# Optimization experiments

Hardware: AMD Instinct MI355X
Metric: run time of the kernel (lower is better)

The kernel has to match this reference:

```python
import jax, jax.numpy as jnp
from jax import lax
import numpy as np

STRIDE = 4
RADIUS = 0.2
NSAMPLE = 32
DENSITY_K = 16
INTRINSIC_DIM = 3
EPS = 1e-8
BN_EPS = 1e-5


def _cdist(a, b):
    # Euclidean pairwise distances: a (..., M, 3), b (..., N, 3) -> (..., M, N)
    d2 = ((a * a).sum(-1)[..., :, None] + (b * b).sum(-1)[..., None, :]
          - 2.0 * jnp.matmul(a, jnp.swapaxes(b, -1, -2)))
    return jnp.sqrt(jnp.maximum(d2, 1e-12))


def _fps(coords, n_samples):
    # iterative farthest point sampling: coords (B, N, 3) -> (B, n_samples) int32
    B, N, _ = coords.shape
    mean = coords.mean(axis=1, keepdims=True)
    farthest = jnp.argmax(((coords - mean) ** 2).sum(-1), axis=1)
    min_dist = jnp.full((B, N), jnp.inf, dtype=coords.dtype)

    def step(carry, _):
        md, far = carry
        centroid = jnp.take_along_axis(coords, far[:, None, None], axis=1)  # (B,1,3)
        d = ((coords - centroid) ** 2).sum(-1)
        md = jnp.minimum(md, d)
        return (md, jnp.argmax(md, axis=1)), far

    _, idxs = lax.scan(step, (min_dist, farthest), None, length=n_samples)
    return idxs.T  # (B, n_samples)


def _ball_query(q, s, radius, k):
    d = _cdist(q, s)  # (B, M, N)
    _, knn_idx = lax.top_k(-d, k)                 # k nearest fallback
    masked = jnp.where(d > radius, jnp.inf, d)
    neg_vals, m_idx = lax.top_k(-masked, k)       # k nearest within radius
    valid = jnp.isfinite(neg_vals)
    return jnp.where(valid, m_idx, knn_idx)


def _density_weights(gc):
    # gc: (B, M, K, 3) -> weights (B, M, K); kth-NN-distance based density weights
    K = gc.shape[2]
    d = _cdist(gc, gc)  # (B, M, K, K)
    d = jnp.where(jnp.eye(K, dtype=bool), jnp.inf, d)
    kk = min(max(DENSITY_K, 1), K - 1)
    kth = -lax.top_k(-d, kk)[0][..., -1]  # distance to kk-th neighbor, (B, M, K)
    raw = jnp.maximum(kth, EPS) ** INTRINSIC_DIM
    return raw / jnp.maximum(raw.sum(axis=-1, keepdims=True), EPS)


def _bn(x, g, b, axes):
    # training-mode batchnorm (biased variance), channel axis = 1
    mu = x.mean(axes, keepdims=True)
    var = x.var(axes, keepdims=True)
    shp = [1] * x.ndim
    shp[1] = -1
    return (x - mu) / jnp.sqrt(var + BN_EPS) * g.reshape(shp) + b.reshape(shp)


def setup_inputs() -> dict:
    key = jax.random.key(0)
    ks = jax.random.split(key, 5)
    B, N, C_in, C_out = 8, 4096, 64, 128
    mid = C_out // 2  # stride > 1 -> mid_channels = out_channels // 2
    coords = jax.random.uniform(ks[0], (B, N, 3), dtype=jnp.float32)
    feats = jax.random.normal(ks[1], (B, C_in, N), dtype=jnp.float32)
    W0 = jax.random.normal(ks[2], (mid, C_in + 3), dtype=jnp.float32) * 0.05
    W1 = jax.random.normal(ks[3], (C_out, mid), dtype=jnp.float32) * 0.05
    Ws = jax.random.normal(ks[4], (C_out, C_in), dtype=jnp.float32) * 0.05
    return {
        "coords": coords, "feats": feats,
        "W0": W0, "g0": jnp.ones((mid,), jnp.float32), "b0": jnp.zeros((mid,), jnp.float32),
        "W1": W1, "g1": jnp.ones((C_out,), jnp.float32), "b1": jnp.zeros((C_out,), jnp.float32),
        "Ws": Ws, "gs": jnp.ones((C_out,), jnp.float32), "bs": jnp.zeros((C_out,), jnp.float32),
    }


def reference(coords, feats, W0, g0, b0, W1, g1, b1, Ws, gs, bs):
    B, N, _ = coords.shape
    M = max(N // STRIDE, 1)
    sample_idx = _fps(coords, M)                               # (B, M)
    gather_pts = jax.vmap(lambda c, i: c[i])                   # (N,3)[idx]
    gather_fts = jax.vmap(lambda f, i: f[:, i])                # (C,N)[:,idx]
    sampled_coords = gather_pts(coords, sample_idx)            # (B, M, 3)
    gidx = _ball_query(sampled_coords, coords, RADIUS, NSAMPLE)  # (B, M, K)
    grouped_coords = gather_pts(coords, gidx)                  # (B, M, K, 3)
    rel = (grouped_coords - sampled_coords[:, :, None, :]) / max(RADIUS, 1e-8)
    grouped_feats = gather_fts(feats, gidx)                    # (B, C_in, M, K)
    x = jnp.concatenate([rel.transpose(0, 3, 1, 2), grouped_feats], axis=1)
    h = jax.nn.relu(_bn(jnp.einsum('oc,bcmk->bomk', W0, x), g0, b0, (0, 2, 3)))
    messages = jax.nn.relu(_bn(jnp.einsum('oc,bcmk->bomk', W1, h), g1, b1, (0, 2, 3)))
    weights = _density_weights(grouped_coords)                 # (B, M, K)
    reduced = (messages * weights[:, None, :, :]).sum(-1)      # (B, C_out, M)
    skip_in = gather_fts(feats, sample_idx)                    # (B, C_in, M)
    skip = _bn(jnp.einsum('oc,bcm->bom', Ws, skip_in), gs, bs, (0, 2))
    return sampled_coords, jax.nn.relu(reduced + skip)
```

## Files before the change

kernel.cpp:

```cpp
#include <hip/hip_runtime.h>
#include <hip/hip_bf16.h>
#include <cstdint>

#define DEV __device__ __forceinline__

constexpr int Bn   = 8;
constexpr int Nn   = 4096;
constexpr int Mn   = 1024;
constexpr int Kn   = 32;
constexpr int CIN  = 64;
constexpr int COUT = 128;

__global__ __launch_bounds__(256) void k_tr(const float* __restrict__ feats,
                                            float* __restrict__ featsT) {
  __shared__ float tile[64][65];
  int b = blockIdx.x >> 6, n0 = (blockIdx.x & 63) * 64;
  int t = threadIdx.x;
  int lane = t & 63, grp = t >> 6;
  for (int r = 0; r < 16; ++r) {
    int c = grp + r * 4;
    tile[c][lane] = feats[((size_t)b * 64 + c) * 4096 + n0 + lane];
  }
  __syncthreads();
  for (int r = 0; r < 16; ++r) {
    int n = grp + r * 4;
    featsT[((size_t)b * 4096 + n0 + n) * 64 + lane] = tile[lane][n];
  }
}

DEV float wave_max_f32(float x) {
#if __has_builtin(__builtin_amdgcn_update_dpp)
#define FSTEP(CTRL, RMASK)                                                      \
  {                                                                             \
    int o = __builtin_amdgcn_update_dpp(0, __float_as_int(x), CTRL, RMASK, 0xf, \
                                        false);                                 \
    x = fmaxf(x, __int_as_float(o));                                            \
  }
  FSTEP(0x111, 0xf)
  FSTEP(0x112, 0xf)
  FSTEP(0x114, 0xf)
  FSTEP(0x118, 0xf)
  FSTEP(0x142, 0xa)
  FSTEP(0x143, 0xc)
#undef FSTEP
#else
  for (int off = 1; off < 64; off <<= 1) x = fmaxf(x, __shfl_xor(x, off, 64));
#endif
  return x;
}

DEV unsigned long long grp8_max_u64(unsigned long long k) {
#if __has_builtin(__builtin_amdgcn_update_dpp)
#define USTEP(CTRL)                                                                    \
  {                                                                                    \
    unsigned int lo = (unsigned int)__builtin_amdgcn_update_dpp(                       \
        0, (int)(unsigned int)k, CTRL, 0xf, 0xf, false);                               \
    unsigned int hi = (unsigned int)__builtin_amdgcn_update_dpp(                       \
        0, (int)(unsigned int)(k >> 32), CTRL, 0xf, 0xf, false);                       \
    unsigned long long o = ((unsigned long long)hi << 32) | lo;                        \
    if (o > k) k = o;                                                                  \
  }
  USTEP(0x111)
  USTEP(0x112)
  USTEP(0x114)
#undef USTEP
#else
  for (int off = 1; off < 8; off <<= 1) {
    unsigned int lo = __shfl_xor((unsigned int)k, off, 64);
    unsigned int hi = __shfl_xor((unsigned int)(k >> 32), off, 64);
    unsigned long long o = ((unsigned long long)hi << 32) | lo;
    if (o > k) k = o;
  }
#endif
  return k;
}

DEV uint32_t fps_round8(const float v[8], int t, unsigned long long (*part)[8], int p) {
  float v4[4]; int j4[4];
#pragma unroll
  for (int i = 0; i < 4; ++i) {
    bool r = v[2 * i + 1] > v[2 * i];
    v4[i] = r ? v[2 * i + 1] : v[2 * i];
    j4[i] = r ? 2 * i + 1 : 2 * i;
  }
  float v2[2]; int j2[2];
#pragma unroll
  for (int i = 0; i < 2; ++i) {
    bool r = v4[2 * i + 1] > v4[2 * i];
    v2[i] = r ? v4[2 * i + 1] : v4[2 * i];
    j2[i] = r ? j4[2 * i + 1] : j4[2 * i];
  }
  bool rr = v2[1] > v2[0];
  float bv = rr ? v2[1] : v2[0];
  int bj = rr ? j2[1] : j2[0];

  float wl = wave_max_f32(bv);
  float wmax = __int_as_float(__builtin_amdgcn_readlane(__float_as_int(wl), 63));
  unsigned long long mask = __ballot(bv == wmax);
  int Ls = (int)__ffsll(mask) - 1;
  int bjw = __shfl(bj, Ls, 64);
  uint32_t idx = 8u * (uint32_t)((t & ~63) + Ls) + (uint32_t)bjw;
  const int sl = p & 1;
  if ((t & 63) == 0)
    part[sl][t >> 6] = ((unsigned long long)__float_as_uint(wmax) << 12) |
                       (unsigned long long)(4095u - idx);
  __syncthreads();
  unsigned long long kk = part[sl][t & 7];
  kk = grp8_max_u64(kk);
  unsigned int lo = (unsigned int)__builtin_amdgcn_readlane((int)(unsigned int)kk, 7);
  return 4095u - (lo & 4095u);
}

__global__ __launch_bounds__(512, 1) void k_fps(const float* __restrict__ coords,
                                                uint32_t* __restrict__ sidx,
                                                float* __restrict__ outc) {
  const int b = blockIdx.x, t = threadIdx.x;
  __shared__ float4 sp[Nn];
  __shared__ unsigned long long part[2][8];
  __shared__ uint32_t farl[Mn];
  __shared__ float s_mean[4];

  const float* cb = coords + (size_t)b * Nn * 3;
  for (int i = t; i < Nn; i += 512)
    sp[i] = make_float4(cb[3 * i], cb[3 * i + 1], cb[3 * i + 2], 0.f);
  __syncthreads();
  if (t == 0) {
    float ax = 0.f, ay = 0.f, az = 0.f;
    for (int i = 0; i < Nn; ++i) {
      float4 c = sp[i];
      ax = __fadd_rn(ax, c.x); ay = __fadd_rn(ay, c.y); az = __fadd_rn(az, c.z);
    }
    s_mean[0] = __fdiv_rn(ax, 4096.f);
    s_mean[1] = __fdiv_rn(ay, 4096.f);
    s_mean[2] = __fdiv_rn(az, 4096.f);
  }
  __syncthreads();

  float px[8], py[8], pz[8], md[8];
#pragma unroll
  for (int j = 0; j < 8; ++j) {
    float4 c = sp[8 * t + j];
    px[j] = c.x; py[j] = c.y; pz[j] = c.z;
    md[j] = __builtin_inff();
  }

  uint32_t far;
  {
    float mx = s_mean[0], my = s_mean[1], mz = s_mean[2];
    float tv[8];
#pragma unroll
    for (int j = 0; j < 8; ++j) {
      float dx = __fsub_rn(px[j], mx), dy = __fsub_rn(py[j], my), dz = __fsub_rn(pz[j], mz);
      tv[j] = __fadd_rn(__fadd_rn(__fmul_rn(dx, dx), __fmul_rn(dy, dy)), __fmul_rn(dz, dz));
    }
    far = fps_round8(tv, t, part, 0);
  }

  for (int p = 1; p < Mn; ++p) {
    if (t == 0) farl[p - 1] = far;
    float4 c = sp[far];
#pragma unroll
    for (int j = 0; j < 8; ++j) {
      float dx = __fsub_rn(px[j], c.x), dy = __fsub_rn(py[j], c.y), dz = __fsub_rn(pz[j], c.z);
      float d = __fadd_rn(__fadd_rn(__fmul_rn(dx, dx), __fmul_rn(dy, dy)), __fmul_rn(dz, dz));
      md[j] = fminf(md[j], d);
    }
    far = fps_round8(md, t, part, p);
  }
  if (t == 0) farl[Mn - 1] = far;
  __syncthreads();

  for (int i = t; i < Mn; i += 512) {
    uint32_t f = farl[i];
    sidx[b * Mn + i] = f;
    float4 c = sp[f];
    outc[(size_t)(b * Mn + i) * 3 + 0] = c.x;
    outc[(size_t)(b * Mn + i) * 3 + 1] = c.y;
    outc[(size_t)(b * Mn + i) * 3 + 2] = c.z;
  }
}

__global__ __launch_bounds__(256) void k_knn(const float* __restrict__ coords,
                                             const uint32_t* __restrict__ sidx,
                                             uint32_t* __restrict__ gidx,
                                             float* __restrict__ wts) {
  const int q = blockIdx.x;
  const int b = q >> 10;
  const int t = threadIdx.x;
  __shared__ unsigned long long keys[Nn + 2];
  __shared__ int s_cnt;
  __shared__ float s_q[4];
  __shared__ uint32_t s_sel[32];
  __shared__ float gx[32], gy[32], gz[32], g2[32];
  __shared__ float dmat[32 * 33];
  __shared__ float kth[32];
  __shared__ float s_raw[32];
  __shared__ float s_sum;

  if (t == 0) {
    uint32_t si = sidx[q];
    const float* c = &coords[((size_t)b * Nn + si) * 3];
    s_q[0] = c[0]; s_q[1] = c[1]; s_q[2] = c[2];
  }
  __syncthreads();
  float qx = s_q[0], qy = s_q[1], qz = s_q[2];
  float q2 = __fadd_rn(__fadd_rn(__fmul_rn(qx, qx), __fmul_rn(qy, qy)), __fmul_rn(qz, qz));
  const float* cb = coords + (size_t)b * Nn * 3;

  float thr = 0.04f;
  int cnt = 0;
  while (true) {
    if (t == 0) s_cnt = 0;
    __syncthreads();
    for (int j = 0; j < 16; ++j) {
      int i = t + 256 * j;
      float cx = cb[3 * i], cy = cb[3 * i + 1], cz = cb[3 * i + 2];
      float c2  = __fadd_rn(__fadd_rn(__fmul_rn(cx, cx), __fmul_rn(cy, cy)), __fmul_rn(cz, cz));
      float dot = __fadd_rn(__fadd_rn(__fmul_rn(qx, cx), __fmul_rn(qy, cy)), __fmul_rn(qz, cz));
      float d2  = __fsub_rn(__fadd_rn(q2, c2), __fmul_rn(2.f, dot));
      float d2c = fmaxf(d2, 1e-12f);
      bool pred = (d2c <= thr);
      unsigned long long mk = __ballot(pred);
      int base = 0;
      if ((t & 63) == 0 && mk) base = atomicAdd(&s_cnt, (int)__popcll(mk));
      base = __shfl(base, 0, 64);
      if (pred) {
        int pos = base + (int)__popcll(mk & ((1ull << (t & 63)) - 1ull));
        keys[pos] = ((unsigned long long)__float_as_uint(d2c) << 32) | (uint32_t)i;
      }
    }
    __syncthreads();
    cnt = s_cnt;
    if (cnt >= 32 || thr > 1.f) break;
    thr = (thr < 0.1f) ? 0.16f : 8.f;
    __syncthreads();
  }
  if (t == 0) { keys[cnt] = ~0ull; keys[cnt + 1] = ~0ull; }
  __syncthreads();
  int cnt2 = (cnt + 1) & ~1;
  for (int i = t; i < cnt; i += 256) {
    unsigned long long ki = keys[i];
    int r = 0;
    for (int j2 = 0; j2 < cnt2; j2 += 2) {
      unsigned long long a = keys[j2], c2 = keys[j2 + 1];
      r += (a < ki) + (c2 < ki);
    }
    if (r < 32) s_sel[r] = (uint32_t)ki;
  }
  __syncthreads();

  if (t < 32) {
    uint32_t gi = s_sel[t];
    gidx[(size_t)q * 32 + t] = gi;
    const float* c = &coords[((size_t)b * Nn + gi) * 3];
    float x = c[0], y = c[1], z = c[2];
    gx[t] = x; gy[t] = y; gz[t] = z;
    g2[t] = __fadd_rn(__fadd_rn(__fmul_rn(x, x), __fmul_rn(y, y)), __fmul_rn(z, z));
  }
  __syncthreads();
  for (int p = t; p < 1024; p += 256) {
    int i = p >> 5, jj = p & 31;
    float dot = __fadd_rn(__fadd_rn(__fmul_rn(gx[i], gx[jj]), __fmul_rn(gy[i], gy[jj])),
                          __fmul_rn(gz[i], gz[jj]));
    float d2 = __fsub_rn(__fadd_rn(g2[i], g2[jj]), __fmul_rn(2.f, dot));
    float dd = sqrtf(fmaxf(d2, 1e-12f));
    if (i == jj) dd = __builtin_inff();
    dmat[i * 33 + jj] = dd;
  }
  __syncthreads();
  for (int p = t; p < 1024; p += 256) {
    int i = p >> 5, jj = p & 31;
    float v = dmat[i * 33 + jj];
    int r = 0;
    for (int c = 0; c < 32; ++c) {
      float u = dmat[i * 33 + c];
      r += (u < v) || (u == v && c < jj);
    }
    if (r == 15) kth[i] = v;
  }
  __syncthreads();
  if (t < 32) { float x = fmaxf(kth[t], 1e-8f); s_raw[t] = x * x * x; }
  __syncthreads();
  if (t == 0) {
    float s = 0.f;
    for (int i2 = 0; i2 < 32; ++i2) s += s_raw[i2];
    s_sum = fmaxf(s, 1e-8f);
  }
  __syncthreads();
  if (t < 32) wts[(size_t)q * 32 + t] = s_raw[t] / s_sum;
}

constexpr int XST = 132;
constexpr int WST = 68;

DEV void build_x(const float* __restrict__ coords, const float* __restrict__ featsT,
                 const uint32_t* __restrict__ sidx, const uint32_t* __restrict__ gidx,
                 const float* __restrict__ W0, int b, int m0, int t,
                 float* xs, float* w0sT, uint32_t* s_gi, float* s_qc) {
  for (int i = t; i < 64 * 67; i += 256) {
    int o = i / 67, c = i - o * 67;
    w0sT[c * WST + o] = W0[i];
  }
  if (t < 128) {
    s_gi[t] = gidx[((size_t)(b * Mn + m0)) * 32 + t];
  } else if (t < 132) {
    int mm = t - 128;
    uint32_t si = sidx[b * Mn + m0 + mm];
    const float* c = &coords[((size_t)b * Nn + si) * 3];
    s_qc[mm * 3 + 0] = c[0]; s_qc[mm * 3 + 1] = c[1]; s_qc[mm * 3 + 2] = c[2];
  }
  __syncthreads();
  if (t < 128) {
    int mm = t >> 5;
    const float* c = &coords[((size_t)b * Nn + s_gi[t]) * 3];
    xs[0 * XST + t] = (c[0] - s_qc[mm * 3 + 0]) / 0.2f;
    xs[1 * XST + t] = (c[1] - s_qc[mm * 3 + 1]) / 0.2f;
    xs[2 * XST + t] = (c[2] - s_qc[mm * 3 + 2]) / 0.2f;
  }
  {
    int c = t & 63, k0g = t >> 6;
    for (int r2 = 0; r2 < 32; ++r2) {
      int kk = k0g + 4 * r2;
      xs[(size_t)(3 + c) * XST + kk] = featsT[((size_t)b * Nn + s_gi[kk]) * 64 + c];
    }
  }
  __syncthreads();
}

DEV void conv1_acc(const float* xs, const float* w0sT, int o0, int k0, float acc[32]) {
#pragma unroll
  for (int i = 0; i < 32; ++i) acc[i] = 0.f;
  for (int c = 0; c < 67; ++c) {
    float4 w  = *(const float4*)&w0sT[c * WST + o0];
    float4 xa = *(const float4*)&xs[c * XST + k0];
    float4 xb = *(const float4*)&xs[c * XST + k0 + 4];
    float wv[4] = {w.x, w.y, w.z, w.w};
    float xv[8] = {xa.x, xa.y, xa.z, xa.w, xb.x, xb.y, xb.z, xb.w};
#pragma unroll
    for (int i = 0; i < 4; ++i)
#pragma unroll
      for (int j = 0; j < 8; ++j)
        acc[i * 8 + j] = fmaf(wv[i], xv[j], acc[i * 8 + j]);
  }
}

DEV void conv2_acc(const float* hs, const float* w1sT, int o0, int k0, float acc2[32]) {
#pragma unroll
  for (int i = 0; i < 32; ++i) acc2[i] = 0.f;
  for (int c = 0; c < 64; ++c) {
    float4 w  = *(const float4*)&w1sT[c * WST + o0];
    float4 xa = *(const float4*)&hs[c * XST + k0];
    float4 xb = *(const float4*)&hs[c * XST + k0 + 4];
    float wv[4] = {w.x, w.y, w.z, w.w};
    float xv[8] = {xa.x, xa.y, xa.z, xa.w, xb.x, xb.y, xb.z, xb.w};
#pragma unroll
    for (int i = 0; i < 4; ++i)
#pragma unroll
      for (int j = 0; j < 8; ++j)
        acc2[i * 8 + j] = fmaf(wv[i], xv[j], acc2[i * 8 + j]);
  }
}

__global__ __launch_bounds__(256) void k_conv1(const float* __restrict__ coords,
                                               const float* __restrict__ featsT,
                                               const uint32_t* __restrict__ sidx,
                                               const uint32_t* __restrict__ gidx,
                                               const float* __restrict__ W0,
                                               float* __restrict__ stats) {
  __shared__ float xs[67 * XST];
  __shared__ float w0sT[67 * WST];
  __shared__ uint32_t s_gi[128];
  __shared__ float s_qc[12];
  __shared__ float ssum[64], ssq[64];
  int blk = blockIdx.x, t = threadIdx.x;
  int b = blk >> 8, m0 = (blk & 255) << 2;
  if (t < 64) { ssum[t] = 0.f; ssq[t] = 0.f; }
  build_x(coords, featsT, sidx, gidx, W0, b, m0, t, xs, w0sT, s_gi, s_qc);
  int o0 = (t & 15) * 4, k0 = (t >> 4) * 8;
  float acc[32];
  conv1_acc(xs, w0sT, o0, k0, acc);
#pragma unroll
  for (int i = 0; i < 4; ++i) {
    float s = 0.f, sq = 0.f;
#pragma unroll
    for (int j = 0; j < 8; ++j) { s += acc[i * 8 + j]; sq = fmaf(acc[i * 8 + j], acc[i * 8 + j], sq); }
    atomicAdd(&ssum[o0 + i], s); atomicAdd(&ssq[o0 + i], sq);
  }
  __syncthreads();
  if (t < 64) { atomicAdd(&stats[t], ssum[t]); atomicAdd(&stats[64 + t], ssq[t]); }
}

__global__ void k_fin0(float* stats, const float* g0, const float* b0) {
  int t = threadIdx.x;
  if (t >= 64) return;
  float mu  = stats[t] * (1.f / 262144.f);
  float var = stats[64 + t] * (1.f / 262144.f) - mu * mu;
  float a = g0[t] / sqrtf(var + 1e-5f);
  stats[640 + t] = a;
  stats[704 + t] = b0[t] - mu * a;
}

__global__ __launch_bounds__(256) void k_conv2(const float* __restrict__ coords,
                                               const float* __restrict__ featsT,
                                               const uint32_t* __restrict__ sidx,
                                               const uint32_t* __restrict__ gidx,
                                               const float* __restrict__ W0,
                                               const float* __restrict__ W1,
                                               float* __restrict__ stats) {
  __shared__ float smU[13400];
  __shared__ uint32_t s_gi[128];
  __shared__ float s_qc[12];
  __shared__ float ssum[128], ssq[128];
  float* xs = smU;  float* w0sT = smU + 67 * XST;
  float* hs = smU;  float* w1sT = smU + 64 * XST;
  int blk = blockIdx.x, t = threadIdx.x;
  int b = blk >> 8, m0 = (blk & 255) << 2;
  if (t < 128) { ssum[t] = 0.f; ssq[t] = 0.f; }
  build_x(coords, featsT, sidx, gidx, W0, b, m0, t, xs, w0sT, s_gi, s_qc);
  int o0 = (t & 15) * 4, k0 = (t >> 4) * 8;
  float acc[32];
  conv1_acc(xs, w0sT, o0, k0, acc);
  float4 a04 = *(const float4*)&stats[640 + o0];
  float4 c04 = *(const float4*)&stats[704 + o0];
  float a0v[4] = {a04.x, a04.y, a04.z, a04.w};
  float c0v[4] = {c04.x, c04.y, c04.z, c04.w};
  __syncthreads();
#pragma unroll
  for (int i = 0; i < 4; ++i) {
    float h[8];
#pragma unroll
    for (int j = 0; j < 8; ++j) h[j] = fmaxf(fmaf(a0v[i], acc[i * 8 + j], c0v[i]), 0.f);
    *(float4*)&hs[(o0 + i) * XST + k0]     = make_float4(h[0], h[1], h[2], h[3]);
    *(float4*)&hs[(o0 + i) * XST + k0 + 4] = make_float4(h[4], h[5], h[6], h[7]);
  }
  for (int p = 0; p < 2; ++p) {
    __syncthreads();
    for (int i = t; i < 64 * 64; i += 256) {
      int oo = i >> 6, cc = i & 63;
      w1sT[cc * WST + oo] = W1[(size_t)(64 * p + oo) * 64 + cc];
    }
    __syncthreads();
    float acc2[32];
    conv2_acc(hs, w1sT, o0, k0, acc2);
#pragma unroll
    for (int i = 0; i < 4; ++i) {
      float s = 0.f, sq = 0.f;
#pragma unroll
      for (int j = 0; j < 8; ++j) { s += acc2[i * 8 + j]; sq = fmaf(acc2[i * 8 + j], acc2[i * 8 + j], sq); }
      atomicAdd(&ssum[64 * p + o0 + i], s); atomicAdd(&ssq[64 * p + o0 + i], sq);
    }
  }
  __syncthreads();
  if (t < 128) { atomicAdd(&stats[128 + t], ssum[t]); atomicAdd(&stats[256 + t], ssq[t]); }
}

__global__ __launch_bounds__(256) void k_skip(const float* __restrict__ featsT,
                                              const uint32_t* __restrict__ sidx,
                                              const float* __restrict__ Ws,
                                              float* __restrict__ ys,
                                              float* __restrict__ stats) {
  __shared__ float fin[64 * 65];
  __shared__ float wssT[64 * 129];
  __shared__ uint32_t s_si[64];
  __shared__ float ssum[128], ssq[128];
  int blk = blockIdx.x, t = threadIdx.x;
  int b = blk >> 4, m0 = (blk & 15) * 64;
  if (t < 64) s_si[t] = sidx[b * Mn + m0 + t];
  if (t < 128) { ssum[t] = 0.f; ssq[t] = 0.f; }
  __syncthreads();
  for (int i = t; i < 64 * 64; i += 256) {
    int mm = i >> 6, c = i & 63;
    fin[mm * 65 + c] = featsT[((size_t)b * Nn + s_si[mm]) * 64 + c];
  }
  for (int i = t; i < 128 * 64; i += 256) {
    int oo = i >> 6, cc = i & 63;
    wssT[cc * 129 + oo] = Ws[(size_t)oo * 64 + cc];
  }
  __syncthreads();
  int o = t & 127, mh = t >> 7;
  float s = 0.f, sq = 0.f;
  for (int mm = mh * 32; mm < mh * 32 + 32; ++mm) {
    float acc = 0.f;
    for (int c = 0; c < 64; ++c) acc = fmaf(wssT[c * 129 + o], fin[mm * 65 + c], acc);
    ys[((size_t)(b * Mn + m0 + mm)) * 128 + o] = acc;
    s += acc; sq = fmaf(acc, acc, sq);
  }
  atomicAdd(&ssum[o], s); atomicAdd(&ssq[o], sq);
  __syncthreads();
  if (t < 128) { atomicAdd(&stats[384 + t], ssum[t]); atomicAdd(&stats[512 + t], ssq[t]); }
}

__global__ void k_fin1(float* stats, const float* g1, const float* b1,
                       const float* gs, const float* bs) {
  int t = threadIdx.x;
  if (t >= 128) return;
  float mu  = stats[128 + t] * (1.f / 262144.f);
  float var = stats[256 + t] * (1.f / 262144.f) - mu * mu;
  float a = g1[t] / sqrtf(var + 1e-5f);
  stats[768 + t] = a;
  stats[896 + t] = b1[t] - mu * a;
  float mus  = stats[384 + t] * (1.f / 8192.f);
  float vars = stats[512 + t] * (1.f / 8192.f) - mus * mus;
  float as = gs[t] / sqrtf(vars + 1e-5f);
  stats[1024 + t] = as;
  stats[1152 + t] = bs[t] - mus * as;
}

__global__ __launch_bounds__(256) void k_out(const float* __restrict__ coords,
                                             const float* __restrict__ featsT,
                                             const uint32_t* __restrict__ sidx,
                                             const uint32_t* __restrict__ gidx,
                                             const float* __restrict__ W0,
                                             const float* __restrict__ W1,
                                             const float* __restrict__ wts,
                                             const float* __restrict__ ys,
                                             const float* __restrict__ stats,
                                             float* __restrict__ out_feat) {
  __shared__ float smU[13400];
  __shared__ uint32_t s_gi[128];
  __shared__ float s_qc[12];
  __shared__ float sw[4 * 36];
  __shared__ float red[128 * 5];
  float* xs = smU;  float* w0sT = smU + 67 * XST;
  float* hs = smU;  float* w1sT = smU + 64 * XST;
  int blk = blockIdx.x, t = threadIdx.x;
  int b = blk >> 8, m0 = (blk & 255) << 2;
  build_x(coords, featsT, sidx, gidx, W0, b, m0, t, xs, w0sT, s_gi, s_qc);
  if (t < 128) sw[(t >> 5) * 36 + (t & 31)] = wts[((size_t)(b * Mn + m0)) * 32 + t];
  int o0 = (t & 15) * 4, k0 = (t >> 4) * 8;
  int m = k0 >> 5, nb0 = k0 & 31;
  float acc[32];
  conv1_acc(xs, w0sT, o0, k0, acc);
  float4 a04 = *(const float4*)&stats[640 + o0];
  float4 c04 = *(const float4*)&stats[704 + o0];
  float a0v[4] = {a04.x, a04.y, a04.z, a04.w};
  float c0v[4] = {c04.x, c04.y, c04.z, c04.w};
  __syncthreads();
#pragma unroll
  for (int i = 0; i < 4; ++i) {
    float h[8];
#pragma unroll
    for (int j = 0; j < 8; ++j) h[j] = fmaxf(fmaf(a0v[i], acc[i * 8 + j], c0v[i]), 0.f);
    *(float4*)&hs[(o0 + i) * XST + k0]     = make_float4(h[0], h[1], h[2], h[3]);
    *(float4*)&hs[(o0 + i) * XST + k0 + 4] = make_float4(h[4], h[5], h[6], h[7]);
  }
  for (int p = 0; p < 2; ++p) {
    __syncthreads();
    for (int i = t; i < 64 * 64; i += 256) {
      int oo = i >> 6, cc = i & 63;
      w1sT[cc * WST + oo] = W1[(size_t)(64 * p + oo) * 64 + cc];
    }
    __syncthreads();
    float acc2[32];
    conv2_acc(hs, w1sT, o0, k0, acc2);
    float4 swa = *(const float4*)&sw[m * 36 + nb0];
    float4 swb = *(const float4*)&sw[m * 36 + nb0 + 4];
    float wv[8] = {swa.x, swa.y, swa.z, swa.w, swb.x, swb.y, swb.z, swb.w};
    float4 a14 = *(const float4*)&stats[768 + 64 * p + o0];
    float4 c14 = *(const float4*)&stats[896 + 64 * p + o0];
    float a1v[4] = {a14.x, a14.y, a14.z, a14.w};
    float c1v[4] = {c14.x, c14.y, c14.z, c14.w};
    float r4[4];
#pragma unroll
    for (int i = 0; i < 4; ++i) {
      float r = 0.f;
#pragma unroll
      for (int j = 0; j < 8; ++j) {
        float msg = fmaxf(fmaf(a1v[i], acc2[i * 8 + j], c1v[i]), 0.f);
        r = fmaf(msg, wv[j], r);
      }
      r4[i] = r;
    }
#pragma unroll
    for (int i = 0; i < 4; ++i) {
      float r = r4[i];
      r += __shfl_xor(r, 16, 64);
      r += __shfl_xor(r, 32, 64);
      r4[i] = r;
    }
    if ((t & 63) < 16) {
      float4 ysv = *(const float4*)&ys[((size_t)(b * Mn + m0 + m)) * 128 + 64 * p + o0];
      float4 as4 = *(const float4*)&stats[1024 + 64 * p + o0];
      float4 cs4 = *(const float4*)&stats[1152 + 64 * p + o0];
      float yv[4] = {ysv.x, ysv.y, ysv.z, ysv.w};
      float av[4] = {as4.x, as4.y, as4.z, as4.w};
      float cv[4] = {cs4.x, cs4.y, cs4.z, cs4.w};
#pragma unroll
      for (int i = 0; i < 4; ++i)
        red[(64 * p + o0 + i) * 5 + m] = fmaxf(r4[i] + fmaf(av[i], yv[i], cv[i]), 0.f);
    }
  }
  __syncthreads();
  for (int e = t; e < 512; e += 256) {
    int oo = e >> 2, mm = e & 3;
    out_feat[(size_t)b * 131072 + (size_t)oo * 1024 + m0 + mm] = red[oo * 5 + mm];
  }
}

extern "C" void kernel_launch(void* const* d_in, const int* in_sizes, int n_in,
                              void* d_out, int out_size, void* d_ws, size_t ws_size,
                              hipStream_t stream) {
  const float* coords = (const float*)d_in[0];
  const float* feats  = (const float*)d_in[1];
  const float* W0 = (const float*)d_in[2];
  const float* g0 = (const float*)d_in[3];
  const float* b0 = (const float*)d_in[4];
  const float* W1 = (const float*)d_in[5];
  const float* g1 = (const float*)d_in[6];
  const float* b1 = (const float*)d_in[7];
  const float* Ws = (const float*)d_in[8];
  const float* gs = (const float*)d_in[9];
  const float* bs = (const float*)d_in[10];

  float* out_coords = (float*)d_out;
  float* out_feat   = out_coords + (size_t)Bn * Mn * 3;

  char* w = (char*)d_ws;
  float*    featsT = (float*)w;    w += (size_t)Bn * Nn * CIN * 4;
  uint32_t* sidx   = (uint32_t*)w; w += (size_t)Bn * Mn * 4;
  uint32_t* gidx   = (uint32_t*)w; w += (size_t)Bn * Mn * Kn * 4;
  float*    wts    = (float*)w;    w += (size_t)Bn * Mn * Kn * 4;
  float*    ys     = (float*)w;    w += (size_t)Bn * Mn * COUT * 4;
  float*    stats  = (float*)w;    w += 1280 * 4;

  hipMemsetAsync(stats, 0, 640 * 4, stream);
  hipLaunchKernelGGL(k_tr,    dim3(512),  dim3(256), 0, stream, feats, featsT);
  hipLaunchKernelGGL(k_fps,   dim3(8),    dim3(512), 0, stream, coords, sidx, out_coords);
  hipLaunchKernelGGL(k_knn,   dim3(8192), dim3(256), 0, stream, coords, sidx, gidx, wts);
  hipLaunchKernelGGL(k_conv1, dim3(2048), dim3(256), 0, stream, coords, featsT, sidx, gidx, W0, stats);
  hipLaunchKernelGGL(k_skip,  dim3(128),  dim3(256), 0, stream, featsT, sidx, Ws, ys, stats);
  hipLaunchKernelGGL(k_fin0,  dim3(1),    dim3(64),  0, stream, stats, g0, b0);
  hipLaunchKernelGGL(k_conv2, dim3(2048), dim3(256), 0, stream, coords, featsT, sidx, gidx, W0, W1, stats);
  hipLaunchKernelGGL(k_fin1,  dim3(1),    dim3(128), 0, stream, stats, g1, b1, gs, bs);
  hipLaunchKernelGGL(k_out,   dim3(2048), dim3(256), 0, stream, coords, featsT, sidx, gidx, W0, W1, wts, ys, stats, out_feat);
}
```

Before: 1.219 ms.

## Morton-sort points in FPS and skip distance updates for far thread bounding balls

The FPS kernel now bucket-sorts each batch's points by a 4-bit-per-axis Morton code, so each thread owns 8 spatially close points. It computes a per-thread bounding sphere and skips the min-distance update and reselection when the new centroid is too far to lower any owned distance. A wave-level __any check can then skip the 64-bit key reduction for whole waves. Ties are broken by original index so the output matches the reference ordering. In exchange it adds sort setup work, a serial prefix sum on one thread, and 64-bit key reductions, while the per-iteration block barrier stays.

```diff
diff --git a/kernel.cpp b/kernel.cpp
--- a/kernel.cpp
+++ b/kernel.cpp
@@ -28,25 +28,40 @@
   }
 }
 
-DEV float wave_max_f32(float x) {
+DEV unsigned long long wave_max_key(unsigned long long key) {
 #if __has_builtin(__builtin_amdgcn_update_dpp)
-#define FSTEP(CTRL, RMASK)                                                      \
-  {                                                                             \
-    int o = __builtin_amdgcn_update_dpp(0, __float_as_int(x), CTRL, RMASK, 0xf, \
-                                        false);                                 \
-    x = fmaxf(x, __int_as_float(o));                                            \
-  }
-  FSTEP(0x111, 0xf)
-  FSTEP(0x112, 0xf)
-  FSTEP(0x114, 0xf)
-  FSTEP(0x118, 0xf)
-  FSTEP(0x142, 0xa)
-  FSTEP(0x143, 0xc)
-#undef FSTEP
+#define DPP_STEP(CTRL, RMASK)                                                          \
+  {                                                                                    \
+    unsigned int lo2 = (unsigned int)__builtin_amdgcn_update_dpp(                      \
+        0, (int)(unsigned int)key, CTRL, RMASK, 0xf, false);                           \
+    unsigned int hi2 = (unsigned int)__builtin_amdgcn_update_dpp(                      \
+        0, (int)(unsigned int)(key >> 32), CTRL, RMASK, 0xf, false);                   \
+    unsigned long long k2 = ((unsigned long long)hi2 << 32) | lo2;                     \
+    if (k2 > key) key = k2;                                                            \
+  }
+  DPP_STEP(0x111, 0xf)
+  DPP_STEP(0x112, 0xf)
+  DPP_STEP(0x114, 0xf)
+  DPP_STEP(0x118, 0xf)
+  DPP_STEP(0x142, 0xa)
+  DPP_STEP(0x143, 0xc)
+#undef DPP_STEP
 #else
-  for (int off = 1; off < 64; off <<= 1) x = fmaxf(x, __shfl_xor(x, off, 64));
+  for (int off = 1; off < 64; off <<= 1) {
+    unsigned int lo2 = __shfl_xor((unsigned int)key, off, 64);
+    unsigned int hi2 = __shfl_xor((unsigned int)(key >> 32), off, 64);
+    unsigned long long k2 = ((unsigned long long)hi2 << 32) | lo2;
+    if (k2 > key) key = k2;
+  }
 #endif
-  return x;
+  return key;
+}
+
+DEV unsigned long long wave_reduce_bcast(unsigned long long key) {
+  key = wave_max_key(key);
+  unsigned int lo = (unsigned int)__builtin_amdgcn_readlane((int)(unsigned int)key, 63);
+  unsigned int hi = (unsigned int)__builtin_amdgcn_readlane((int)(unsigned int)(key >> 32), 63);
+  return ((unsigned long long)hi << 32) | lo;
 }
 
 DEV unsigned long long grp8_max_u64(unsigned long long k) {
@@ -75,59 +90,65 @@
   return k;
 }
 
-DEV uint32_t fps_round8(const float v[8], int t, unsigned long long (*part)[8], int p) {
-  float v4[4]; int j4[4];
+DEV void tree8_idx(const float v[8], const int oid[8], int sbase,
+                   float& bv, int& bo, int& bs) {
+  float v4[4]; int o4[4], s4[4];
 #pragma unroll
   for (int i = 0; i < 4; ++i) {
-    bool r = v[2 * i + 1] > v[2 * i];
-    v4[i] = r ? v[2 * i + 1] : v[2 * i];
-    j4[i] = r ? 2 * i + 1 : 2 * i;
-  }
-  float v2[2]; int j2[2];
+    int a = 2 * i, c = 2 * i + 1;
+    bool r = (v[c] > v[a]) || (v[c] == v[a] && oid[c] < oid[a]);
+    v4[i] = r ? v[c] : v[a]; o4[i] = r ? oid[c] : oid[a]; s4[i] = sbase + (r ? c : a);
+  }
+  float v2[2]; int o2[2], s2[2];
 #pragma unroll
   for (int i = 0; i < 2; ++i) {
-    bool r = v4[2 * i + 1] > v4[2 * i];
-    v2[i] = r ? v4[2 * i + 1] : v4[2 * i];
-    j2[i] = r ? j4[2 * i + 1] : j4[2 * i];
-  }
-  bool rr = v2[1] > v2[0];
-  float bv = rr ? v2[1] : v2[0];
-  int bj = rr ? j2[1] : j2[0];
-
-  float wl = wave_max_f32(bv);
-  float wmax = __int_as_float(__builtin_amdgcn_readlane(__float_as_int(wl), 63));
-  unsigned long long mask = __ballot(bv == wmax);
-  int Ls = (int)__ffsll(mask) - 1;
-  int bjw = __shfl(bj, Ls, 64);
-  uint32_t idx = 8u * (uint32_t)((t & ~63) + Ls) + (uint32_t)bjw;
-  const int sl = p & 1;
-  if ((t & 63) == 0)
-    part[sl][t >> 6] = ((unsigned long long)__float_as_uint(wmax) << 12) |
-                       (unsigned long long)(4095u - idx);
-  __syncthreads();
-  unsigned long long kk = part[sl][t & 7];
-  kk = grp8_max_u64(kk);
-  unsigned int lo = (unsigned int)__builtin_amdgcn_readlane((int)(unsigned int)kk, 7);
-  return 4095u - (lo & 4095u);
+    int a = 2 * i, c = 2 * i + 1;
+    bool r = (v4[c] > v4[a]) || (v4[c] == v4[a] && o4[c] < o4[a]);
+    v2[i] = r ? v4[c] : v4[a]; o2[i] = r ? o4[c] : o4[a]; s2[i] = r ? s4[c] : s4[a];
+  }
+  bool r = (v2[1] > v2[0]) || (v2[1] == v2[0] && o2[1] < o2[0]);
+  bv = r ? v2[1] : v2[0]; bo = r ? o2[1] : o2[0]; bs = r ? s2[1] : s2[0];
+}
+
+DEV int expand3(int v) {
+  return (v & 1) | ((v & 2) << 2) | ((v & 4) << 4) | ((v & 8) << 6);
+}
+DEV int mcode(float x, float y, float z) {
+  int ix = min(15, max(0, (int)(x * 16.f)));
+  int iy = min(15, max(0, (int)(y * 16.f)));
+  int iz = min(15, max(0, (int)(z * 16.f)));
+  return expand3(ix) | (expand3(iy) << 1) | (expand3(iz) << 2);
+}
+
+DEV unsigned long long pack_key(float bv, int bo, int bs) {
+  return ((unsigned long long)__float_as_uint(bv) << 24) |
+         ((unsigned long long)(4095 - bo) << 12) | (unsigned long long)bs;
 }
 
 __global__ __launch_bounds__(512, 1) void k_fps(const float* __restrict__ coords,
                                                 uint32_t* __restrict__ sidx,
                                                 float* __restrict__ outc) {
   const int b = blockIdx.x, t = threadIdx.x;
-  __shared__ float4 sp[Nn];
+  __shared__ float4 spA[Nn];
+  __shared__ float4 spS[Nn];
+  __shared__ int    hist[Nn];
   __shared__ unsigned long long part[2][8];
   __shared__ uint32_t farl[Mn];
   __shared__ float s_mean[4];
 
   const float* cb = coords + (size_t)b * Nn * 3;
   for (int i = t; i < Nn; i += 512)
-    sp[i] = make_float4(cb[3 * i], cb[3 * i + 1], cb[3 * i + 2], 0.f);
-  __syncthreads();
+    spA[i] = make_float4(cb[3 * i], cb[3 * i + 1], cb[3 * i + 2], 0.f);
+  for (int i = t; i < Nn; i += 512) hist[i] = 0;
+  __syncthreads();
+  for (int i = t; i < Nn; i += 512) {
+    float4 c = spA[i];
+    atomicAdd(&hist[mcode(c.x, c.y, c.z)], 1);
+  }
   if (t == 0) {
     float ax = 0.f, ay = 0.f, az = 0.f;
     for (int i = 0; i < Nn; ++i) {
-      float4 c = sp[i];
+      float4 c = spA[i];
       ax = __fadd_rn(ax, c.x); ay = __fadd_rn(ay, c.y); az = __fadd_rn(az, c.z);
     }
     s_mean[0] = __fdiv_rn(ax, 4096.f);
@@ -135,16 +156,52 @@
     s_mean[2] = __fdiv_rn(az, 4096.f);
   }
   __syncthreads();
-
-  float px[8], py[8], pz[8], md[8];
+  int lc[8]; int lsum = 0;
+#pragma unroll
+  for (int j = 0; j < 8; ++j) { lc[j] = hist[8 * t + j]; lsum += lc[j]; }
+  farl[t] = (uint32_t)lsum;
+  __syncthreads();
+  if (t == 0) {
+    int run = 0;
+    for (int j = 0; j < 512; ++j) { int v = (int)farl[j]; farl[j] = (uint32_t)run; run += v; }
+  }
+  __syncthreads();
+  {
+    int base = (int)farl[t];
+#pragma unroll
+    for (int j = 0; j < 8; ++j) { hist[8 * t + j] = base; base += lc[j]; }
+  }
+  __syncthreads();
+  for (int i = t; i < Nn; i += 512) {
+    float4 c = spA[i];
+    int pos = atomicAdd(&hist[mcode(c.x, c.y, c.z)], 1);
+    spS[pos] = make_float4(c.x, c.y, c.z, __int_as_float(i));
+  }
+  __syncthreads();
+
+  float px[8], py[8], pz[8], md[8]; int oid[8];
 #pragma unroll
   for (int j = 0; j < 8; ++j) {
-    float4 c = sp[8 * t + j];
+    float4 c = spS[8 * t + j];
     px[j] = c.x; py[j] = c.y; pz[j] = c.z;
+    oid[j] = __float_as_int(c.w);
     md[j] = __builtin_inff();
   }
-
-  uint32_t far;
+  float bcx = 0.f, bcy = 0.f, bcz = 0.f;
+#pragma unroll
+  for (int j = 0; j < 8; ++j) { bcx += px[j]; bcy += py[j]; bcz += pz[j]; }
+  bcx *= 0.125f; bcy *= 0.125f; bcz *= 0.125f;
+  float rr = 0.f;
+#pragma unroll
+  for (int j = 0; j < 8; ++j) {
+    float dx = px[j] - bcx, dy = py[j] - bcy, dz = pz[j] - bcz;
+    rr = fmaxf(rr, dx * dx + dy * dy + dz * dz);
+  }
+  const float rad = sqrtf(rr) * 1.0001f + 1e-3f;
+  float s_skip = __builtin_inff();
+  unsigned long long ckey, wkey;
+
+  uint32_t lo_win;
   {
     float mx = s_mean[0], my = s_mean[1], mz = s_mean[2];
     float tv[8];
@@ -153,27 +210,56 @@
       float dx = __fsub_rn(px[j], mx), dy = __fsub_rn(py[j], my), dz = __fsub_rn(pz[j], mz);
       tv[j] = __fadd_rn(__fadd_rn(__fmul_rn(dx, dx), __fmul_rn(dy, dy)), __fmul_rn(dz, dz));
     }
-    far = fps_round8(tv, t, part, 0);
+    float bv; int bo, bs;
+    tree8_idx(tv, oid, 8 * t, bv, bo, bs);
+    ckey = pack_key(bv, bo, bs);
+    wkey = wave_reduce_bcast(ckey);
+    if ((t & 63) == 0) part[0][t >> 6] = wkey;
+    __syncthreads();
+    unsigned long long kk = part[0][t & 7];
+    kk = grp8_max_u64(kk);
+    lo_win = (uint32_t)__builtin_amdgcn_readlane((int)(unsigned int)kk, 7);
   }
 
   for (int p = 1; p < Mn; ++p) {
-    if (t == 0) farl[p - 1] = far;
-    float4 c = sp[far];
-#pragma unroll
-    for (int j = 0; j < 8; ++j) {
-      float dx = __fsub_rn(px[j], c.x), dy = __fsub_rn(py[j], c.y), dz = __fsub_rn(pz[j], c.z);
-      float d = __fadd_rn(__fadd_rn(__fmul_rn(dx, dx), __fmul_rn(dy, dy)), __fmul_rn(dz, dz));
-      md[j] = fminf(md[j], d);
-    }
-    far = fps_round8(md, t, part, p);
-  }
-  if (t == 0) farl[Mn - 1] = far;
+    if (t == 0)
+      farl[p - 1] = (4095u - ((lo_win >> 12) & 4095u)) | ((lo_win & 4095u) << 12);
+    float4 c = spS[lo_win & 4095u];
+    float dxc = c.x - bcx, dyc = c.y - bcy, dzc = c.z - bcz;
+    float D2 = dxc * dxc + dyc * dyc + dzc * dzc;
+    bool upd = (D2 < s_skip);
+    if (__any((int)upd)) {
+      if (upd) {
+#pragma unroll
+        for (int j = 0; j < 8; ++j) {
+          float dx = __fsub_rn(px[j], c.x), dy = __fsub_rn(py[j], c.y), dz = __fsub_rn(pz[j], c.z);
+          float d = __fadd_rn(__fadd_rn(__fmul_rn(dx, dx), __fmul_rn(dy, dy)), __fmul_rn(dz, dz));
+          md[j] = fminf(md[j], d);
+        }
+        float bv; int bo, bs;
+        tree8_idx(md, oid, 8 * t, bv, bo, bs);
+        ckey = pack_key(bv, bo, bs);
+        float sv = sqrtf(bv) + rad;
+        s_skip = sv * sv;
+      }
+      wkey = wave_reduce_bcast(ckey);
+    }
+    const int sl = p & 1;
+    if ((t & 63) == 0) part[sl][t >> 6] = wkey;
+    __syncthreads();
+    unsigned long long kk = part[sl][t & 7];
+    kk = grp8_max_u64(kk);
+    lo_win = (uint32_t)__builtin_amdgcn_readlane((int)(unsigned int)kk, 7);
+  }
+  if (t == 0)
+    farl[Mn - 1] = (4095u - ((lo_win >> 12) & 4095u)) | ((lo_win & 4095u) << 12);
   __syncthreads();
 
   for (int i = t; i < Mn; i += 512) {
     uint32_t f = farl[i];
-    sidx[b * Mn + i] = f;
-    float4 c = sp[f];
+    uint32_t oidx = f & 4095u, spos = (f >> 12) & 4095u;
+    sidx[b * Mn + i] = oidx;
+    float4 c = spS[spos];
     outc[(size_t)(b * Mn + i) * 3 + 0] = c.x;
     outc[(size_t)(b * Mn + i) * 3 + 1] = c.y;
     outc[(size_t)(b * Mn + i) * 3 + 2] = c.z;
```

Result: slower. 2.131 ms (+74.8%).

## Cache conv1 pre-activations in bf16, fuse transpose into FPS launch

Applied to the files above, without the earlier changes.

Conv1 outputs are now written once to a bf16 workspace buffer. The conv2-stats and output kernels read that buffer instead of rebuilding the gathered input and recomputing conv1 in each pass. The BN finalize kernels are folded into the consumers, and the feats transpose runs as extra blocks of the FPS launch so it can overlap with the 8-block FPS. This trades extra memory traffic (32MB written and read twice) and bf16 rounding of the intermediate for removing redundant gather and GEMM work. The cached path only runs when the workspace is large enough.

```diff
diff --git a/kernel.cpp b/kernel.cpp
--- a/kernel.cpp
+++ b/kernel.cpp
@@ -10,23 +10,6 @@
 constexpr int Kn   = 32;
 constexpr int CIN  = 64;
 constexpr int COUT = 128;
-
-__global__ __launch_bounds__(256) void k_tr(const float* __restrict__ feats,
-                                            float* __restrict__ featsT) {
-  __shared__ float tile[64][65];
-  int b = blockIdx.x >> 6, n0 = (blockIdx.x & 63) * 64;
-  int t = threadIdx.x;
-  int lane = t & 63, grp = t >> 6;
-  for (int r = 0; r < 16; ++r) {
-    int c = grp + r * 4;
-    tile[c][lane] = feats[((size_t)b * 64 + c) * 4096 + n0 + lane];
-  }
-  __syncthreads();
-  for (int r = 0; r < 16; ++r) {
-    int n = grp + r * 4;
-    featsT[((size_t)b * 4096 + n0 + n) * 64 + lane] = tile[lane][n];
-  }
-}
 
 DEV float wave_max_f32(float x) {
 #if __has_builtin(__builtin_amdgcn_update_dpp)
@@ -111,15 +94,36 @@
   return 4095u - (lo & 4095u);
 }
 
-__global__ __launch_bounds__(512, 1) void k_fps(const float* __restrict__ coords,
-                                                uint32_t* __restrict__ sidx,
-                                                float* __restrict__ outc) {
-  const int b = blockIdx.x, t = threadIdx.x;
-  __shared__ float4 sp[Nn];
+__global__ __launch_bounds__(512, 1) void k_fused(const float* __restrict__ coords,
+                                                  const float* __restrict__ feats,
+                                                  float* __restrict__ featsT,
+                                                  uint32_t* __restrict__ sidx,
+                                                  float* __restrict__ outc) {
+  __shared__ __align__(16) char smraw[Nn * 16];
   __shared__ unsigned long long part[2][8];
   __shared__ uint32_t farl[Mn];
   __shared__ float s_mean[4];
-
+  const int t = threadIdx.x;
+
+  if (blockIdx.x >= 8) {
+    float (*tile)[65] = (float(*)[65])smraw;
+    int bid = blockIdx.x - 8;
+    int b = bid >> 6, n0 = (bid & 63) * 64;
+    int lane = t & 63, grp = t >> 6;
+    for (int r = 0; r < 8; ++r) {
+      int c = grp + r * 8;
+      tile[c][lane] = feats[((size_t)b * 64 + c) * 4096 + n0 + lane];
+    }
+    __syncthreads();
+    for (int r = 0; r < 8; ++r) {
+      int n = grp + r * 8;
+      featsT[((size_t)b * 4096 + n0 + n) * 64 + lane] = tile[lane][n];
+    }
+    return;
+  }
+
+  float4* sp = (float4*)smraw;
+  const int b = blockIdx.x;
   const float* cb = coords + (size_t)b * Nn * 3;
   for (int i = t; i < Nn; i += 512)
     sp[i] = make_float4(cb[3 * i], cb[3 * i + 1], cb[3 * i + 2], 0.f);
@@ -366,7 +370,8 @@
                                                const uint32_t* __restrict__ sidx,
                                                const uint32_t* __restrict__ gidx,
                                                const float* __restrict__ W0,
-                                               float* __restrict__ stats) {
+                                               float* __restrict__ stats,
+                                               unsigned short* __restrict__ accb) {
   __shared__ float xs[67 * XST];
   __shared__ float w0sT[67 * WST];
   __shared__ uint32_t s_gi[128];
@@ -379,6 +384,23 @@
   int o0 = (t & 15) * 4, k0 = (t >> 4) * 8;
   float acc[32];
   conv1_acc(xs, w0sT, o0, k0, acc);
+  if (accb != nullptr) {
+    unsigned short* at = accb + (size_t)blk * 8192;
+#pragma unroll
+    for (int i = 0; i < 4; ++i) {
+      unsigned int w[4];
+#pragma unroll
+      for (int q = 0; q < 4; ++q) {
+        __hip_bfloat16 h0 = __float2bfloat16(acc[i * 8 + 2 * q]);
+        __hip_bfloat16 h1 = __float2bfloat16(acc[i * 8 + 2 * q + 1]);
+        unsigned short u0 = *reinterpret_cast<unsigned short*>(&h0);
+        unsigned short u1 = *reinterpret_cast<unsigned short*>(&h1);
+        w[q] = (unsigned int)u0 | ((unsigned int)u1 << 16);
+      }
+      uint4 v = make_uint4(w[0], w[1], w[2], w[3]);
+      *(uint4*)&at[(o0 + i) * 128 + k0] = v;
+    }
+  }
 #pragma unroll
   for (int i = 0; i < 4; ++i) {
     float s = 0.f, sq = 0.f;
@@ -388,6 +410,166 @@
   }
   __syncthreads();
   if (t < 64) { atomicAdd(&stats[t], ssum[t]); atomicAdd(&stats[64 + t], ssq[t]); }
+}
+
+__global__ __launch_bounds__(256) void k_conv2c(const unsigned short* __restrict__ accb,
+                                                const float* __restrict__ W1,
+                                                float* __restrict__ stats,
+                                                const float* __restrict__ g0,
+                                                const float* __restrict__ b0) {
+  __shared__ float hs[64 * XST];
+  __shared__ float w1sT[64 * WST];
+  __shared__ float s_a0[64], s_c0[64];
+  __shared__ float ssum[128], ssq[128];
+  int blk = blockIdx.x, t = threadIdx.x;
+  if (t < 128) { ssum[t] = 0.f; ssq[t] = 0.f; }
+  if (t < 64) {
+    float mu  = stats[t] * (1.f / 262144.f);
+    float var = stats[64 + t] * (1.f / 262144.f) - mu * mu;
+    float a = g0[t] / sqrtf(var + 1e-5f);
+    s_a0[t] = a; s_c0[t] = b0[t] - mu * a;
+  }
+  const unsigned short* at = accb + (size_t)blk * 8192;
+  int o = t >> 2, kb = (t & 3) * 32;
+  __syncthreads();
+  float a0 = s_a0[o], c0 = s_c0[o];
+#pragma unroll
+  for (int g = 0; g < 4; ++g) {
+    uint4 v = *(const uint4*)&at[o * 128 + kb + 8 * g];
+    unsigned int vv[4] = {v.x, v.y, v.z, v.w};
+#pragma unroll
+    for (int q = 0; q < 4; ++q) {
+      float f0 = __uint_as_float((vv[q] & 0xffffu) << 16);
+      float f1 = __uint_as_float(vv[q] & 0xffff0000u);
+      hs[o * XST + kb + 8 * g + 2 * q]     = fmaxf(fmaf(a0, f0, c0), 0.f);
+      hs[o * XST + kb + 8 * g + 2 * q + 1] = fmaxf(fmaf(a0, f1, c0), 0.f);
+    }
+  }
+  int o0 = (t & 15) * 4, k0 = (t >> 4) * 8;
+  for (int p = 0; p < 2; ++p) {
+    __syncthreads();
+    for (int i = t; i < 64 * 64; i += 256) {
+      int oo = i >> 6, cc = i & 63;
+      w1sT[cc * WST + oo] = W1[(size_t)(64 * p + oo) * 64 + cc];
+    }
+    __syncthreads();
+    float acc2[32];
+    conv2_acc(hs, w1sT, o0, k0, acc2);
+#pragma unroll
+    for (int i = 0; i < 4; ++i) {
+      float s = 0.f, sq = 0.f;
+#pragma unroll
+      for (int j = 0; j < 8; ++j) { s += acc2[i * 8 + j]; sq = fmaf(acc2[i * 8 + j], acc2[i * 8 + j], sq); }
+      atomicAdd(&ssum[64 * p + o0 + i], s); atomicAdd(&ssq[64 * p + o0 + i], sq);
+    }
+  }
+  __syncthreads();
+  if (t < 128) { atomicAdd(&stats[128 + t], ssum[t]); atomicAdd(&stats[256 + t], ssq[t]); }
+}
+
+__global__ __launch_bounds__(256) void k_outc(const unsigned short* __restrict__ accb,
+                                              const float* __restrict__ W1,
+                                              const float* __restrict__ wts,
+                                              const float* __restrict__ ys,
+                                              const float* __restrict__ stats,
+                                              const float* __restrict__ g0,
+                                              const float* __restrict__ b0,
+                                              const float* __restrict__ g1,
+                                              const float* __restrict__ b1,
+                                              const float* __restrict__ gs,
+                                              const float* __restrict__ bs,
+                                              float* __restrict__ out_feat) {
+  __shared__ float hs[64 * XST];
+  __shared__ float w1sT[64 * WST];
+  __shared__ float s_a0[64], s_c0[64];
+  __shared__ float s_a1[128], s_c1[128], s_as[128], s_cs[128];
+  __shared__ __align__(16) float sw[4 * 36];
+  __shared__ float red[128 * 5];
+  int blk = blockIdx.x, t = threadIdx.x;
+  int b = blk >> 8, m0 = (blk & 255) << 2;
+  if (t < 64) {
+    float mu  = stats[t] * (1.f / 262144.f);
+    float var = stats[64 + t] * (1.f / 262144.f) - mu * mu;
+    float a = g0[t] / sqrtf(var + 1e-5f);
+    s_a0[t] = a; s_c0[t] = b0[t] - mu * a;
+  }
+  if (t < 128) {
+    float mu  = stats[128 + t] * (1.f / 262144.f);
+    float var = stats[256 + t] * (1.f / 262144.f) - mu * mu;
+    float a = g1[t] / sqrtf(var + 1e-5f);
+    s_a1[t] = a; s_c1[t] = b1[t] - mu * a;
+    float mus  = stats[384 + t] * (1.f / 8192.f);
+    float vars = stats[512 + t] * (1.f / 8192.f) - mus * mus;
+    float as = gs[t] / sqrtf(vars + 1e-5f);
+    s_as[t] = as; s_cs[t] = bs[t] - mus * as;
+    sw[(t >> 5) * 36 + (t & 31)] = wts[((size_t)(b * Mn + m0)) * 32 + t];
+  }
+  const unsigned short* at = accb + (size_t)blk * 8192;
+  int o = t >> 2, kb = (t & 3) * 32;
+  __syncthreads();
+  float a0 = s_a0[o], c0 = s_c0[o];
+#pragma unroll
+  for (int g = 0; g < 4; ++g) {
+    uint4 v = *(const uint4*)&at[o * 128 + kb + 8 * g];
+    unsigned int vv[4] = {v.x, v.y, v.z, v.w};
+#pragma unroll
+    for (int q = 0; q < 4; ++q) {
+      float f0 = __uint_as_float((vv[q] & 0xffffu) << 16);
+      float f1 = __uint_as_float(vv[q] & 0xffff0000u);
+      hs[o * XST + kb + 8 * g + 2 * q]     = fmaxf(fmaf(a0, f0, c0), 0.f);
+      hs[o * XST + kb + 8 * g + 2 * q + 1] = fmaxf(fmaf(a0, f1, c0), 0.f);
+    }
+  }
+  int o0 = (t & 15) * 4, k0 = (t >> 4) * 8;
+  int m = k0 >> 5, nb0 = k0 & 31;
+  for (int p = 0; p < 2; ++p) {
+    __syncthreads();
+    for (int i = t; i < 64 * 64; i += 256) {
+      int oo = i >> 6, cc = i & 63;
+      w1sT[cc * WST + oo] = W1[(size_t)(64 * p + oo) * 64 + cc];
+    }
+    __syncthreads();
+    float acc2[32];
+    conv2_acc(hs, w1sT, o0, k0, acc2);
+    float4 swa = *(const float4*)&sw[m * 36 + nb0];
+    float4 swb = *(const float4*)&sw[m * 36 + nb0 + 4];
+    float wv[8] = {swa.x, swa.y, swa.z, swa.w, swb.x, swb.y, swb.z, swb.w};
+    float a1v[4], c1v[4];
+#pragma unroll
+    for (int i = 0; i < 4; ++i) { a1v[i] = s_a1[64 * p + o0 + i]; c1v[i] = s_c1[64 * p + o0 + i]; }
+    float r4[4];
+#pragma unroll
+    for (int i = 0; i < 4; ++i) {
+      float r = 0.f;
+#pragma unroll
+      for (int j = 0; j < 8; ++j) {
+        float msg = fmaxf(fmaf(a1v[i], acc2[i * 8 + j], c1v[i]), 0.f);
+        r = fmaf(msg, wv[j], r);
+      }
+      r4[i] = r;
+    }
+#pragma unroll
+    for (int i = 0; i < 4; ++i) {
+      float r = r4[i];
+      r += __shfl_xor(r, 16, 64);
+      r += __shfl_xor(r, 32, 64);
+      r4[i] = r;
+    }
+    if ((t & 63) < 16) {
+      float4 ysv = *(const float4*)&ys[((size_t)(b * Mn + m0 + m)) * 128 + 64 * p + o0];
+      float yv[4] = {ysv.x, ysv.y, ysv.z, ysv.w};
+#pragma unroll
+      for (int i = 0; i < 4; ++i) {
+        int o2 = 64 * p + o0 + i;
+        red[o2 * 5 + m] = fmaxf(r4[i] + fmaf(s_as[o2], yv[i], s_cs[o2]), 0.f);
+      }
+    }
+  }
+  __syncthreads();
+  for (int e = t; e < 512; e += 256) {
+    int oo = e >> 2, mm = e & 3;
+    out_feat[(size_t)b * 131072 + (size_t)oo * 1024 + m0 + mm] = red[oo * 5 + mm];
+  }
 }
 
 __global__ void k_fin0(float* stats, const float* g0, const float* b0) {
@@ -519,7 +701,7 @@
   __shared__ float smU[13400];
   __shared__ uint32_t s_gi[128];
   __shared__ float s_qc[12];
-  __shared__ float sw[4 * 36];
+  __shared__ __align__(16) float sw[4 * 36];
   __shared__ float red[128 * 5];
   float* xs = smU;  float* w0sT = smU + 67 * XST;
   float* hs = smU;  float* w1sT = smU + 64 * XST;
@@ -621,16 +803,28 @@
   uint32_t* gidx   = (uint32_t*)w; w += (size_t)Bn * Mn * Kn * 4;
   float*    wts    = (float*)w;    w += (size_t)Bn * Mn * Kn * 4;
   float*    ys     = (float*)w;    w += (size_t)Bn * Mn * COUT * 4;
+  unsigned short* accb = (unsigned short*)w; w += (size_t)2048 * 8192 * 2;
   float*    stats  = (float*)w;    w += 1280 * 4;
+  const bool cachemode = ws_size >= (size_t)(w - (char*)d_ws);
 
   hipMemsetAsync(stats, 0, 640 * 4, stream);
-  hipLaunchKernelGGL(k_tr,    dim3(512),  dim3(256), 0, stream, feats, featsT);
-  hipLaunchKernelGGL(k_fps,   dim3(8),    dim3(512), 0, stream, coords, sidx, out_coords);
+  hipLaunchKernelGGL(k_fused, dim3(520),  dim3(512), 0, stream,
+                     coords, feats, featsT, sidx, out_coords);
   hipLaunchKernelGGL(k_knn,   dim3(8192), dim3(256), 0, stream, coords, sidx, gidx, wts);
-  hipLaunchKernelGGL(k_conv1, dim3(2048), dim3(256), 0, stream, coords, featsT, sidx, gidx, W0, stats);
+  hipLaunchKernelGGL(k_conv1, dim3(2048), dim3(256), 0, stream,
+                     coords, featsT, sidx, gidx, W0, stats,
+                     cachemode ? accb : (unsigned short*)nullptr);
   hipLaunchKernelGGL(k_skip,  dim3(128),  dim3(256), 0, stream, featsT, sidx, Ws, ys, stats);
-  hipLaunchKernelGGL(k_fin0,  dim3(1),    dim3(64),  0, stream, stats, g0, b0);
-  hipLaunchKernelGGL(k_conv2, dim3(2048), dim3(256), 0, stream, coords, featsT, sidx, gidx, W0, W1, stats);
-  hipLaunchKernelGGL(k_fin1,  dim3(1),    dim3(128), 0, stream, stats, g1, b1, gs, bs);
-  hipLaunchKernelGGL(k_out,   dim3(2048), dim3(256), 0, stream, coords, featsT, sidx, gidx, W0, W1, wts, ys, stats, out_feat);
-}
+  if (cachemode) {
+    hipLaunchKernelGGL(k_conv2c, dim3(2048), dim3(256), 0, stream, accb, W1, stats, g0, b0);
+    hipLaunchKernelGGL(k_outc,   dim3(2048), dim3(256), 0, stream,
+                       accb, W1, wts, ys, stats, g0, b0, g1, b1, gs, bs, out_feat);
+  } else {
+    hipLaunchKernelGGL(k_fin0,  dim3(1),    dim3(64),  0, stream, stats, g0, b0);
+    hipLaunchKernelGGL(k_conv2, dim3(2048), dim3(256), 0, stream,
+                       coords, featsT, sidx, gidx, W0, W1, stats);
+    hipLaunchKernelGGL(k_fin1,  dim3(1),    dim3(128), 0, stream, stats, g1, b1, gs, bs);
+    hipLaunchKernelGGL(k_out,   dim3(2048), dim3(256), 0, stream,
+                       coords, featsT, sidx, gidx, W0, W1, wts, ys, stats, out_feat);
+  }
+}
```

Result: faster. 1.100 ms (-9.8%).
